# Kernel tuning notes

Hardware: AMD Instinct MI355X
Metric: run time of the kernel (lower is better)

The kernel has to match this reference:

```python
import jax, jax.numpy as jnp
import numpy as np

N, D_IN, D_EMB, K = 16384, 1024, 256, 1024
ALPHA, EPS = 0.01, 1e-5


def setup_inputs() -> dict:
    key = jax.random.key(0)
    ks = jax.random.split(key, 6)
    inp = jax.random.normal(ks[0], (N, D_IN), dtype=jnp.float32)
    W_send = jax.random.normal(ks[1], (D_IN, D_EMB), dtype=jnp.float32) / np.sqrt(D_IN)
    b_send = jnp.zeros((D_EMB,), dtype=jnp.float32)
    W_recv = jax.random.normal(ks[2], (D_EMB, D_IN), dtype=jnp.float32) / np.sqrt(D_EMB)
    b_recv = jnp.zeros((D_IN,), dtype=jnp.float32)
    codebook = jax.random.normal(ks[3], (K, D_EMB), dtype=jnp.float32)
    ema_vecs = codebook.copy()
    ema_size = jnp.zeros((K,), dtype=jnp.float32)
    return {"input": inp, "W_send": W_send, "b_send": b_send,
            "W_recv": W_recv, "b_recv": b_recv, "codebook": codebook,
            "ema_vecs": ema_vecs, "ema_size": ema_size}


def reference(input, W_send, b_send, W_recv, b_recv, codebook, ema_vecs, ema_size):
    sg = jax.lax.stop_gradient
    # send projection -> latent z  [N, D_EMB]
    z = input @ W_send + b_send
    # nearest-neighbor lookup: argmin_k ||e_k||^2 - 2 <z, e_k>
    sqr = jnp.sum(codebook * codebook, axis=1)          # [K]
    cov = jnp.einsum('nj,kj->nk', z, codebook)          # [N, K]
    codes = jnp.argmin(sqr - 2.0 * cov, axis=-1)        # [N] int
    # fetch embeddings (gather)
    vectors = codebook[codes]                            # [N, D_EMB]
    # mse losses, reduction='sum'
    embedding = jnp.sum((vectors - sg(z)) ** 2)
    commitment = jnp.sum((z - sg(vectors)) ** 2)
    # straight-through output
    emb_out = z + sg(vectors - z)
    # EMA accumulate (one-hot scatter == segment_sum)
    upd_vecs = jax.ops.segment_sum(z, codes, num_segments=K)              # [K, D_EMB]
    upd_size = jax.ops.segment_sum(jnp.ones((z.shape[0],), z.dtype), codes, num_segments=K)
    ema_vecs_new = ema_vecs + ALPHA * (upd_vecs - ema_vecs)
    ema_size_new = ema_size + ALPHA * (upd_size - ema_size)
    # EMA update (Laplace-smoothed centroid)
    n = jnp.sum(ema_size_new)
    coef = n / (n + K * EPS)
    size = coef * (ema_size_new + EPS)
    weight_new = ema_vecs_new / size[:, None]
    # empirical entropy of the codes in bits
    prob = jnp.bincount(codes, length=K).astype(jnp.float32) / codes.size
    ent = -jnp.sum(jnp.where(prob > 0, prob * jnp.log(prob), 0.0)) / jnp.log(2.0)
    # recv projection
    x = emb_out @ W_recv + b_recv
    return (x, codes, embedding, commitment, ent, ema_vecs_new, ema_size_new, weight_new)
```

## Files before the change

### kernel.cpp

```cpp
#include <hip/hip_runtime.h>
#include <math.h>

#define NROWS 16384
#define DIN   1024
#define DEMB  256
#define KC    1024
#define ALPHA 0.01f
#define EPSV  1e-5f
#define INV2048 4.8828125e-4f
#define CHUNK 32
#define COV_CHUNKS 8

typedef _Float16 f16;
typedef __attribute__((ext_vector_type(4)))  _Float16 f16x4;
typedef __attribute__((ext_vector_type(8)))  _Float16 f16x8;
typedef __attribute__((ext_vector_type(16))) float    f32x16;
typedef unsigned long long u64;

#define OFF_Z       0
#define OFF_R       4194304
#define OFF_SQR     5242880
#define OFF_ZH      5243904
#define OFF_ZL      7341056
#define OFF_WTH     9438208
#define OFF_WTL     9569280
#define OFF_CBH     9700352
#define OFF_CBL     9831424
#define OFF_KEYS    9962496
#define OFF_CODES   9995264
#define OFF_LIST    10011648
#define OFF_OFFS    10028032
#define OFF_UPD     10029056
#define OFF_HIST    10291200
#define OFF_CURSOR  10292224
#define OFF_LOSS    10293248
#define ZERO_LEN    264208
#define OFF_COUNTSF 10293264
#define OFF_SIZE    10294288

#define OUT_X      0
#define OUT_CODES  16777216
#define OUT_EMB    16793600
#define OUT_COMMIT 16793601
#define OUT_ENT    16793602
#define OUT_EMAV   16793603
#define OUT_EMAS   17055747
#define OUT_W      17056771

__device__ __forceinline__ void split_f32(float x, f16& h, f16& l) {
    h = (f16)x;
    l = (f16)((x - (float)h) * 2048.0f);
}

__global__ __launch_bounds__(64) void sqr_kernel(const float* __restrict__ cb,
                                                 float* __restrict__ sqr) {
    int k = blockIdx.x;
    int lane = threadIdx.x;
    float4 v = ((const float4*)cb)[k * 64 + lane];
    float s = v.x * v.x + v.y * v.y + v.z * v.z + v.w * v.w;
    for (int off = 32; off > 0; off >>= 1) s += __shfl_down(s, off, 64);
    if (lane == 0) sqr[k] = s;
}

__global__ __launch_bounds__(256) void split_wt_kernel(const float* __restrict__ W,
                                                       f16* __restrict__ wth,
                                                       f16* __restrict__ wtl) {
    int n = blockIdx.x;
    int t = threadIdx.x;
    f16x4 h4, l4;
#pragma unroll
    for (int j = 0; j < 4; ++j) {
        int k = t * 4 + j;
        float x = W[(size_t)k * DEMB + n];
        f16 h, l; split_f32(x, h, l);
        h4[j] = h; l4[j] = l;
    }
    *(f16x4*)&wth[(size_t)n * DIN + t * 4] = h4;
    *(f16x4*)&wtl[(size_t)n * DIN + t * 4] = l4;
}

__global__ __launch_bounds__(256) void split_cb_kernel(const float* __restrict__ cb,
                                                       f16* __restrict__ cbh,
                                                       f16* __restrict__ cbl) {
    int idx = (blockIdx.x * 256 + threadIdx.x) * 4;
    float4 v = *(const float4*)&cb[idx];
    f16x4 h4, l4;
    f16 h, l;
    split_f32(v.x, h, l); h4[0] = h; l4[0] = l;
    split_f32(v.y, h, l); h4[1] = h; l4[1] = l;
    split_f32(v.z, h, l); h4[2] = h; l4[2] = l;
    split_f32(v.w, h, l); h4[3] = h; l4[3] = l;
    *(f16x4*)&cbh[idx] = h4;
    *(f16x4*)&cbl[idx] = l4;
}

__global__ __launch_bounds__(512) void gemm1_mfma(const float* __restrict__ in,
                                                  const f16* __restrict__ wth,
                                                  const f16* __restrict__ wtl,
                                                  const float* __restrict__ bsend,
                                                  float* __restrict__ z,
                                                  f16* __restrict__ zh,
                                                  f16* __restrict__ zl) {
    __shared__ f16 sm[2 * 2 * 2 * 128 * 64];
    const int tid = threadIdx.x;
    const int wave = tid >> 6, lane = tid & 63;
    const int half = lane >> 5, l31 = lane & 31;
    const int wrow = wave >> 2, wcol = wave & 3;
    const int rowBase = blockIdx.y * 128;
    const int colBase = blockIdx.x * 128;

    const int sr  = tid >> 2;
    const int skq = tid & 3;
    const int sr7 = sr & 7;

    f32x16 accm[2] = {};
    f32x16 accx[2] = {};

    auto stageB = [&](int buf, int ks) {
#pragma unroll
        for (int i = 0; i < 4; ++i) {
            const int q  = wave * 4 + i;
            const int hl = q >> 4;
            const int c  = (q & 15) * 8 + (lane >> 3);
            const int p  = lane & 7;
            const int s  = p ^ (c & 7);
            const f16* src = (hl ? wtl : wth)
                           + (size_t)(colBase + c) * DIN + ks + s * 8;
            f16* dst = sm + buf * 32768 + 16384 + q * 512 + lane * 8;
            __builtin_amdgcn_global_load_lds(
                (const __attribute__((address_space(1))) void*)src,
                (__attribute__((address_space(3))) void*)dst, 16, 0, 0);
        }
    };

    auto loadA = [&](int ks, float4* av) {
        const float* src = &in[(size_t)(rowBase + sr) * DIN + ks + skq * 16];
#pragma unroll
        for (int j = 0; j < 4; ++j) av[j] = ((const float4*)src)[j];
    };

    auto writeA = [&](int buf, const float4* av) {
        f16* Abase = sm + buf * 32768;
#pragma unroll
        for (int q = 0; q < 2; ++q) {
            f16x8 h8, l8;
#pragma unroll
            for (int j = 0; j < 2; ++j) {
                float4 v = av[q * 2 + j];
                f16 h, l;
                split_f32(v.x, h, l); h8[j * 4 + 0] = h; l8[j * 4 + 0] = l;
                split_f32(v.y, h, l); h8[j * 4 + 1] = h; l8[j * 4 + 1] = l;
                split_f32(v.z, h, l); h8[j * 4 + 2] = h; l8[j * 4 + 2] = l;
                split_f32(v.w, h, l); h8[j * 4 + 3] = h; l8[j * 4 + 3] = l;
            }
            const int s = skq * 2 + q;
            const int off = sr * 64 + ((s ^ sr7) << 3);
            *(f16x8*)&Abase[off] = h8;
            *(f16x8*)&Abase[8192 + off] = l8;
        }
    };

    auto compute = [&](int buf) {
        const f16* Ah = sm + buf * 32768;
        const f16* Al = Ah + 8192;
        const f16* Bh = Ah + 16384;
        const f16* Bl = Ah + 24576;
        const int c  = wcol * 32 + l31;
        const int c7 = c & 7;
#pragma unroll
        for (int t4 = 0; t4 < 4; ++t4) {
            const int s = t4 * 2 + half;
            f16x8 a_h[2], a_l[2];
#pragma unroll
            for (int rt = 0; rt < 2; ++rt) {
                const int r = wrow * 64 + rt * 32 + l31;
                const int off = r * 64 + ((s ^ (r & 7)) << 3);
                a_h[rt] = *(const f16x8*)&Ah[off];
                a_l[rt] = *(const f16x8*)&Al[off];
            }
            const int boff = c * 64 + ((s ^ c7) << 3);
            f16x8 b_h = *(const f16x8*)&Bh[boff];
            f16x8 b_l = *(const f16x8*)&Bl[boff];
#pragma unroll
            for (int rt = 0; rt < 2; ++rt) {
                accm[rt] = __builtin_amdgcn_mfma_f32_32x32x16_f16(a_h[rt], b_h, accm[rt], 0, 0, 0);
                accx[rt] = __builtin_amdgcn_mfma_f32_32x32x16_f16(a_h[rt], b_l, accx[rt], 0, 0, 0);
                accx[rt] = __builtin_amdgcn_mfma_f32_32x32x16_f16(a_l[rt], b_h, accx[rt], 0, 0, 0);
            }
        }
    };

    stageB(0, 0);
    {
        float4 av[4];
        loadA(0, av);
        writeA(0, av);
    }
    __syncthreads();

    int cur = 0;
    for (int step = 0; step < 16; ++step) {
        float4 av[4];
        const bool pf = (step + 1) < 16;
        if (pf) {
            stageB(cur ^ 1, (step + 1) * 64);
            loadA((step + 1) * 64, av);
        }
        compute(cur);
        if (pf) writeA(cur ^ 1, av);
        __syncthreads();
        cur ^= 1;
    }

#pragma unroll
    for (int rt = 0; rt < 2; ++rt) {
        const int col = colBase + wcol * 32 + l31;
        const float bb = bsend[col];
#pragma unroll
        for (int reg = 0; reg < 16; ++reg) {
            const int row = rowBase + wrow * 64 + rt * 32 + (reg & 3) + 8 * (reg >> 2) + 4 * half;
            const float zv = accm[rt][reg] + INV2048 * accx[rt][reg] + bb;
            const size_t o = (size_t)row * DEMB + col;
            z[o] = zv;
            f16 h = (f16)zv;
            zh[o] = h;
            zl[o] = (f16)((zv - (float)h) * 2048.0f);
        }
    }
}

__device__ __forceinline__ void cov_stage(const f16* __restrict__ cbh,
                                          const f16* __restrict__ cbl,
                                          f16* sC, int buf, int codeBase,
                                          int wave, int lane) {
#pragma unroll
    for (int i = 0; i < 8; ++i) {
        const int seg = wave * 8 + i;
        const int hl  = seg >> 4;
        const int rp  = seg & 15;
        const int r   = rp * 2 + (lane >> 5);
        const f16* src = (hl ? cbl : cbh)
                       + (size_t)(codeBase + r) * DEMB
                       + (((lane & 31) ^ r) << 3);
        f16* dst = sC + (((buf << 1) + hl) * 32 + rp * 2) * DEMB;
        __builtin_amdgcn_global_load_lds(
            (const __attribute__((address_space(1))) void*)src,
            (__attribute__((address_space(3))) void*)dst,
            16, 0, 0);
    }
}

__global__ __launch_bounds__(256, 2) void cov_mfma_kernel(const f16* __restrict__ zh,
                                                          const f16* __restrict__ zl,
                                                          const f16* __restrict__ cbh,
                                                          const f16* __restrict__ cbl,
                                                          const float* __restrict__ sqr,
                                                          u64* __restrict__ keys) {
    __shared__ f16 sC[2 * 2 * 32 * DEMB];
    const int tid = threadIdx.x;
    const int wave = tid >> 6, lane = tid & 63;
    const int half = lane >> 5, l31 = lane & 31;
    const int rowBase = blockIdx.y * 128 + wave * 32;
    const int myRow = rowBase + l31;
    const int cb0 = blockIdx.x * (COV_CHUNKS * 32);

    cov_stage(cbh, cbl, sC, 0, cb0, wave, lane);

    f16x8 a_h[16], a_l[16];
#pragma unroll
    for (int t = 0; t < 16; ++t) {
        size_t o = (size_t)myRow * DEMB + t * 16 + half * 8;
        a_h[t] = *(const f16x8*)&zh[o];
        a_l[t] = *(const f16x8*)&zl[o];
    }

    float runv[16];
    int   runc[16];
#pragma unroll
    for (int r = 0; r < 16; ++r) { runv[r] = 3.4e38f; runc[r] = 0; }

    for (int cc = 0; cc < COV_CHUNKS; ++cc) {
        __syncthreads();
        if (cc + 1 < COV_CHUNKS)
            cov_stage(cbh, cbl, sC, (cc + 1) & 1, cb0 + (cc + 1) * 32, wave, lane);

        const f16* Ch = sC + ((cc & 1) * 2 + 0) * 32 * DEMB;
        const f16* Cl = sC + ((cc & 1) * 2 + 1) * 32 * DEMB;

        f32x16 accm = {};
        f32x16 accx = {};
#pragma unroll
        for (int t = 0; t < 16; ++t) {
            const int seg = t * 2 + half;
            const int p = ((seg ^ l31) << 3);
            f16x8 b_h = *(const f16x8*)&Ch[l31 * DEMB + p];
            f16x8 b_l = *(const f16x8*)&Cl[l31 * DEMB + p];
            accm = __builtin_amdgcn_mfma_f32_32x32x16_f16(a_h[t], b_h, accm, 0, 0, 0);
            accx = __builtin_amdgcn_mfma_f32_32x32x16_f16(a_h[t], b_l, accx, 0, 0, 0);
            accx = __builtin_amdgcn_mfma_f32_32x32x16_f16(a_l[t], b_h, accx, 0, 0, 0);
        }

        const int code = cb0 + cc * 32 + l31;
        const float sqv = sqr[code];
#pragma unroll
        for (int r = 0; r < 16; ++r) {
            float s = sqv - 2.0f * (accm[r] + INV2048 * accx[r]);
            if (s < runv[r]) { runv[r] = s; runc[r] = code; }
        }
    }

#pragma unroll
    for (int r = 0; r < 16; ++r) {
        float v = runv[r]; int ci = runc[r];
        for (int off = 16; off > 0; off >>= 1) {
            float ov = __shfl_down(v, off, 32);
            int   oc = __shfl_down(ci, off, 32);
            if (ov < v || (ov == v && oc < ci)) { v = ov; ci = oc; }
        }
        if (l31 == 0) {
            int row = rowBase + (r & 3) + 8 * (r >> 2) + 4 * half;
            unsigned ub = __float_as_uint(v);
            ub = (ub & 0x80000000u) ? ~ub : (ub | 0x80000000u);
            u64 key = ((u64)ub << 32) | (unsigned)ci;
            atomicMin(&keys[row], key);
        }
    }
}

__global__ __launch_bounds__(256) void decode_kernel(const u64* __restrict__ keys,
                                                     int* __restrict__ codes,
                                                     float* __restrict__ out_codes,
                                                     int* __restrict__ hist) {
    int r = blockIdx.x * 256 + threadIdx.x;
    int c = (int)(keys[r] & 0xFFFFFFFFull);
    codes[r] = c;
    out_codes[r] = (float)c;
    atomicAdd(&hist[c], 1);
}

__global__ __launch_bounds__(1024) void prefix_kernel(const int* __restrict__ hist,
                                                      int* __restrict__ offs,
                                                      float* __restrict__ countsf) {
    __shared__ int s[1024];
    int t = threadIdx.x;
    int v = hist[t];
    s[t] = v;
    countsf[t] = (float)v;
    __syncthreads();
    for (int d = 1; d < 1024; d <<= 1) {
        int x = (t >= d) ? s[t - d] : 0;
        __syncthreads();
        s[t] += x;
        __syncthreads();
    }
    offs[t] = s[t] - v;
}

__global__ __launch_bounds__(256) void fill_kernel(const int* __restrict__ codes,
                                                   const int* __restrict__ offs,
                                                   int* __restrict__ cursor,
                                                   int* __restrict__ list) {
    int r = blockIdx.x * 256 + threadIdx.x;
    int c = codes[r];
    int pos = offs[c] + atomicAdd(&cursor[c], 1);
    list[pos] = r;
}

__global__ __launch_bounds__(256) void upd_loss_kernel(const float* __restrict__ z,
                                                       const float* __restrict__ cb,
                                                       const int* __restrict__ list,
                                                       const int* __restrict__ codes,
                                                       float* __restrict__ upd,
                                                       float* __restrict__ loss) {
    __shared__ int srow[CHUNK];
    __shared__ int scode[CHUNK];
    const int tid = threadIdx.x;
    const int base = blockIdx.x * CHUNK;
    if (tid < CHUNK) {
        int r = list[base + tid];
        srow[tid] = r;
        scode[tid] = codes[r];
    }
    __syncthreads();

    int cur = scode[0];
    float cbv = cb[(size_t)cur * DEMB + tid];
    float acc = 0.f, lacc = 0.f;
    float zv = z[(size_t)srow[0] * DEMB + tid];
#pragma unroll 4
    for (int i = 0; i < CHUNK; ++i) {
        float znext = (i + 1 < CHUNK) ? z[(size_t)srow[i + 1] * DEMB + tid] : 0.f;
        int c = scode[i];
        if (c != cur) {
            atomicAdd(&upd[(size_t)cur * DEMB + tid], acc);
            acc = 0.f;
            cur = c;
            cbv = cb[(size_t)cur * DEMB + tid];
        }
        acc += zv;
        float d = zv - cbv;
        lacc += d * d;
        zv = znext;
    }
    atomicAdd(&upd[(size_t)cur * DEMB + tid], acc);

    __shared__ float red[256];
    red[tid] = lacc;
    __syncthreads();
    for (int s = 128; s > 0; s >>= 1) {
        if (tid < s) red[tid] += red[tid + s];
        __syncthreads();
    }
    if (tid == 0) atomicAdd(loss, red[0]);
}

__global__ __launch_bounds__(256) void gemm64_kernel(const float* __restrict__ A,
                                                     const float* __restrict__ B,
                                                     float* __restrict__ C,
                                                     int M, int Kd, int Nc) {
    __shared__ float As[16][68];
    __shared__ float Bs[16][64];
    const int tid = threadIdx.x;
    const int tx = tid & 15, ty = tid >> 4;
    const int rowBase = blockIdx.y * 64;
    const int colBase = blockIdx.x * 64;

    float acc[4][4];
#pragma unroll
    for (int i = 0; i < 4; ++i)
#pragma unroll
        for (int j = 0; j < 4; ++j) acc[i][j] = 0.f;

    const int a_row = tid >> 2;
    const int a_c4  = (tid & 3) * 4;
    const int b_r   = tid >> 4;
    const int b_c4  = (tid & 15) * 4;

    for (int kk = 0; kk < Kd; kk += 16) {
        float4 av = *(const float4*)&A[(size_t)(rowBase + a_row) * Kd + kk + a_c4];
        float4 bv = *(const float4*)&B[(size_t)(kk + b_r) * Nc + colBase + b_c4];
        __syncthreads();
        As[a_c4 + 0][a_row] = av.x;  As[a_c4 + 1][a_row] = av.y;
        As[a_c4 + 2][a_row] = av.z;  As[a_c4 + 3][a_row] = av.w;
        *(float4*)&Bs[b_r][b_c4] = bv;
        __syncthreads();
#pragma unroll
        for (int d = 0; d < 16; ++d) {
            float4 a01 = *(const float4*)&As[d][ty * 4];
            float4 b01 = *(const float4*)&Bs[d][tx * 4];
            float a[4] = {a01.x, a01.y, a01.z, a01.w};
            float b[4] = {b01.x, b01.y, b01.z, b01.w};
#pragma unroll
            for (int i = 0; i < 4; ++i)
#pragma unroll
                for (int j = 0; j < 4; ++j) acc[i][j] += a[i] * b[j];
        }
    }

#pragma unroll
    for (int i = 0; i < 4; ++i) {
        int r = rowBase + ty * 4 + i;
        *(float4*)&C[(size_t)r * Nc + colBase + tx * 4] =
            make_float4(acc[i][0], acc[i][1], acc[i][2], acc[i][3]);
    }
}

__global__ __launch_bounds__(256) void recv_kernel(const float* __restrict__ R,
                                                   const float* __restrict__ brecv,
                                                   const int* __restrict__ codes,
                                                   float* __restrict__ out) {
    const int n = blockIdx.x;
    const int t = threadIdx.x;
    const int code = codes[n];
    float4 r = ((const float4*)(R + (size_t)code * DIN))[t];
    float4 b = ((const float4*)brecv)[t];
    ((float4*)(out + (size_t)n * DIN))[t] =
        make_float4(r.x + b.x, r.y + b.y, r.z + b.z, r.w + b.w);
}

__global__ __launch_bounds__(1024) void ema_small_kernel(const float* __restrict__ ema_size,
                                                         const float* __restrict__ counts,
                                                         const float* __restrict__ loss,
                                                         float* __restrict__ size_ws,
                                                         float* __restrict__ out) {
    __shared__ float rn[1024];
    __shared__ float re[1024];
    const int k = threadIdx.x;
    float c  = counts[k];
    float es = ema_size[k];
    float esn = es + ALPHA * (c - es);
    out[OUT_EMAS + k] = esn;
    float p = c * (1.0f / (float)NROWS);
    rn[k] = esn;
    re[k] = (p > 0.f) ? p * logf(p) : 0.f;
    __syncthreads();
    for (int s = 512; s > 0; s >>= 1) {
        if (k < s) { rn[k] += rn[k + s]; re[k] += re[k + s]; }
        __syncthreads();
    }
    float n = rn[0];
    float coef = n / (n + (float)KC * EPSV);
    size_ws[k] = coef * (esn + EPSV);
    if (k == 0) {
        out[OUT_ENT] = -re[0] / logf(2.0f);
        float l = loss[0];
        out[OUT_EMB] = l;
        out[OUT_COMMIT] = l;
    }
}

__global__ __launch_bounds__(256) void emav_kernel(const float* __restrict__ ema_vecs,
                                                   const float* __restrict__ upd,
                                                   const float* __restrict__ size_ws,
                                                   float* __restrict__ out) {
    int idx = blockIdx.x * 256 + threadIdx.x;
    float ev = ema_vecs[idx], uv = upd[idx];
    float evn = ev + ALPHA * (uv - ev);
    out[OUT_EMAV + idx] = evn;
    out[OUT_W + idx] = evn / size_ws[idx >> 8];
}

extern "C" void kernel_launch(void* const* d_in, const int* in_sizes, int n_in,
                              void* d_out, int out_size, void* d_ws, size_t ws_size,
                              hipStream_t stream) {
    const float* input    = (const float*)d_in[0];
    const float* W_send   = (const float*)d_in[1];
    const float* b_send   = (const float*)d_in[2];
    const float* W_recv   = (const float*)d_in[3];
    const float* b_recv   = (const float*)d_in[4];
    const float* codebook = (const float*)d_in[5];
    const float* ema_vecs = (const float*)d_in[6];
    const float* ema_size = (const float*)d_in[7];
    float* out = (float*)d_out;
    float* ws  = (float*)d_ws;
    int*   wsi = (int*)d_ws;

    f16* wth = (f16*)(ws + OFF_WTH);
    f16* wtl = (f16*)(ws + OFF_WTL);
    f16* cbh = (f16*)(ws + OFF_CBH);
    f16* cbl = (f16*)(ws + OFF_CBL);
    f16* zh  = (f16*)(ws + OFF_ZH);
    f16* zl  = (f16*)(ws + OFF_ZL);
    u64* keys = (u64*)(ws + OFF_KEYS);

    (void)hipMemsetAsync(ws + OFF_UPD, 0, (size_t)ZERO_LEN * sizeof(float), stream);
    (void)hipMemsetAsync(ws + OFF_KEYS, 0xFF, (size_t)NROWS * sizeof(u64), stream);

    sqr_kernel<<<KC, 64, 0, stream>>>(codebook, ws + OFF_SQR);
    split_wt_kernel<<<DEMB, 256, 0, stream>>>(W_send, wth, wtl);
    split_cb_kernel<<<256, 256, 0, stream>>>(codebook, cbh, cbl);

    gemm64_kernel<<<dim3(DIN / 64, KC / 64), 256, 0, stream>>>(
        codebook, W_recv, ws + OFF_R, KC, DEMB, DIN);

    gemm1_mfma<<<dim3(DEMB / 128, NROWS / 128), 512, 0, stream>>>(
        input, wth, wtl, b_send, ws + OFF_Z, zh, zl);

    cov_mfma_kernel<<<dim3(KC / (COV_CHUNKS * 32), NROWS / 128), 256, 0, stream>>>(
        zh, zl, cbh, cbl, ws + OFF_SQR, keys);

    decode_kernel<<<NROWS / 256, 256, 0, stream>>>(
        keys, wsi + OFF_CODES, out + OUT_CODES, wsi + OFF_HIST);

    prefix_kernel<<<1, 1024, 0, stream>>>(
        wsi + OFF_HIST, wsi + OFF_OFFS, ws + OFF_COUNTSF);

    fill_kernel<<<NROWS / 256, 256, 0, stream>>>(
        wsi + OFF_CODES, wsi + OFF_OFFS, wsi + OFF_CURSOR, wsi + OFF_LIST);

    upd_loss_kernel<<<NROWS / CHUNK, 256, 0, stream>>>(
        ws + OFF_Z, codebook, wsi + OFF_LIST, wsi + OFF_CODES,
        ws + OFF_UPD, ws + OFF_LOSS);

    recv_kernel<<<NROWS, 256, 0, stream>>>(
        ws + OFF_R, b_recv, wsi + OFF_CODES, out + OUT_X);

    ema_small_kernel<<<1, 1024, 0, stream>>>(
        ema_size, ws + OFF_COUNTSF, ws + OFF_LOSS, ws + OFF_SIZE, out);

    emav_kernel<<<KC, 256, 0, stream>>>(
        ema_vecs, ws + OFF_UPD, ws + OFF_SIZE, out);
}
```

Before: 277.3 us.

## Retile send-projection GEMM to 64x128 blocks with 32-wide K steps

The first split-fp16 MFMA GEMM now uses 64-row by 128-column blocks of 256 threads, with K steps of 32 instead of 64. Shared memory per block shrinks and launch bounds request two blocks per CU, so more blocks are resident and the grid has twice as many blocks to spread load. The LDS swizzle changes from XOR to a rotate-by-row scheme to fit the narrower rows. The cost is twice as many pipeline steps and barriers, and less B-tile reuse per block. The cov kernel edit multiplies a term by zero and changes nothing.

```diff
diff --git a/kernel.cpp b/kernel.cpp
--- a/kernel.cpp
+++ b/kernel.cpp
@@ -94,24 +94,22 @@
     *(f16x4*)&cbl[idx] = l4;
 }
 
-__global__ __launch_bounds__(512) void gemm1_mfma(const float* __restrict__ in,
-                                                  const f16* __restrict__ wth,
-                                                  const f16* __restrict__ wtl,
-                                                  const float* __restrict__ bsend,
-                                                  float* __restrict__ z,
-                                                  f16* __restrict__ zh,
-                                                  f16* __restrict__ zl) {
-    __shared__ f16 sm[2 * 2 * 2 * 128 * 64];
+__global__ __launch_bounds__(256, 2) void gemm1_mfma(const float* __restrict__ in,
+                                                     const f16* __restrict__ wth,
+                                                     const f16* __restrict__ wtl,
+                                                     const float* __restrict__ bsend,
+                                                     float* __restrict__ z,
+                                                     f16* __restrict__ zh,
+                                                     f16* __restrict__ zl) {
+    __shared__ f16 sm[2 * 12288];
     const int tid = threadIdx.x;
     const int wave = tid >> 6, lane = tid & 63;
     const int half = lane >> 5, l31 = lane & 31;
-    const int wrow = wave >> 2, wcol = wave & 3;
-    const int rowBase = blockIdx.y * 128;
+    const int rowBase = blockIdx.y * 64;
     const int colBase = blockIdx.x * 128;
 
     const int sr  = tid >> 2;
     const int skq = tid & 3;
-    const int sr7 = sr & 7;
 
     f32x16 accm[2] = {};
     f32x16 accx[2] = {};
@@ -120,13 +118,14 @@
 #pragma unroll
         for (int i = 0; i < 4; ++i) {
             const int q  = wave * 4 + i;
-            const int hl = q >> 4;
-            const int c  = (q & 15) * 8 + (lane >> 3);
-            const int p  = lane & 7;
-            const int s  = p ^ (c & 7);
+            const int hl = q >> 3;
+            const int c0 = (q & 7) * 16;
+            const int c  = c0 + (lane >> 2);
+            const int p  = lane & 3;
+            const int s  = (p - (c >> 1)) & 3;
             const f16* src = (hl ? wtl : wth)
-                           + (size_t)(colBase + c) * DIN + ks + s * 8;
-            f16* dst = sm + buf * 32768 + 16384 + q * 512 + lane * 8;
+                           + (size_t)(colBase + c) * DIN + ks + (s << 3);
+            f16* dst = sm + buf * 12288 + 4096 + hl * 4096 + c0 * 32;
             __builtin_amdgcn_global_load_lds(
                 (const __attribute__((address_space(1))) void*)src,
                 (__attribute__((address_space(3))) void*)dst, 16, 0, 0);
@@ -134,51 +133,47 @@
     };
 
     auto loadA = [&](int ks, float4* av) {
-        const float* src = &in[(size_t)(rowBase + sr) * DIN + ks + skq * 16];
-#pragma unroll
-        for (int j = 0; j < 4; ++j) av[j] = ((const float4*)src)[j];
+        const float* src = &in[(size_t)(rowBase + sr) * DIN + ks + skq * 8];
+        av[0] = ((const float4*)src)[0];
+        av[1] = ((const float4*)src)[1];
     };
 
     auto writeA = [&](int buf, const float4* av) {
-        f16* Abase = sm + buf * 32768;
-#pragma unroll
-        for (int q = 0; q < 2; ++q) {
-            f16x8 h8, l8;
-#pragma unroll
-            for (int j = 0; j < 2; ++j) {
-                float4 v = av[q * 2 + j];
-                f16 h, l;
-                split_f32(v.x, h, l); h8[j * 4 + 0] = h; l8[j * 4 + 0] = l;
-                split_f32(v.y, h, l); h8[j * 4 + 1] = h; l8[j * 4 + 1] = l;
-                split_f32(v.z, h, l); h8[j * 4 + 2] = h; l8[j * 4 + 2] = l;
-                split_f32(v.w, h, l); h8[j * 4 + 3] = h; l8[j * 4 + 3] = l;
-            }
-            const int s = skq * 2 + q;
-            const int off = sr * 64 + ((s ^ sr7) << 3);
-            *(f16x8*)&Abase[off] = h8;
-            *(f16x8*)&Abase[8192 + off] = l8;
-        }
+        f16x8 h8, l8;
+        f16 h, l;
+        split_f32(av[0].x, h, l); h8[0] = h; l8[0] = l;
+        split_f32(av[0].y, h, l); h8[1] = h; l8[1] = l;
+        split_f32(av[0].z, h, l); h8[2] = h; l8[2] = l;
+        split_f32(av[0].w, h, l); h8[3] = h; l8[3] = l;
+        split_f32(av[1].x, h, l); h8[4] = h; l8[4] = l;
+        split_f32(av[1].y, h, l); h8[5] = h; l8[5] = l;
+        split_f32(av[1].z, h, l); h8[6] = h; l8[6] = l;
+        split_f32(av[1].w, h, l); h8[7] = h; l8[7] = l;
+        const int p = (skq + (sr >> 1)) & 3;
+        const int off = sr * 32 + (p << 3);
+        f16* Abase = sm + buf * 12288;
+        *(f16x8*)&Abase[off] = h8;
+        *(f16x8*)&Abase[2048 + off] = l8;
     };
 
     auto compute = [&](int buf) {
-        const f16* Ah = sm + buf * 32768;
-        const f16* Al = Ah + 8192;
-        const f16* Bh = Ah + 16384;
-        const f16* Bl = Ah + 24576;
-        const int c  = wcol * 32 + l31;
-        const int c7 = c & 7;
-#pragma unroll
-        for (int t4 = 0; t4 < 4; ++t4) {
-            const int s = t4 * 2 + half;
+        const f16* Ah = sm + buf * 12288;
+        const f16* Al = Ah + 2048;
+        const f16* Bh = Ah + 4096;
+        const f16* Bl = Ah + 8192;
+        const int c = wave * 32 + l31;
+#pragma unroll
+        for (int t = 0; t < 2; ++t) {
+            const int s = t * 2 + half;
             f16x8 a_h[2], a_l[2];
 #pragma unroll
             for (int rt = 0; rt < 2; ++rt) {
-                const int r = wrow * 64 + rt * 32 + l31;
-                const int off = r * 64 + ((s ^ (r & 7)) << 3);
+                const int r = rt * 32 + l31;
+                const int off = r * 32 + ((((s + (r >> 1)) & 3)) << 3);
                 a_h[rt] = *(const f16x8*)&Ah[off];
                 a_l[rt] = *(const f16x8*)&Al[off];
             }
-            const int boff = c * 64 + ((s ^ c7) << 3);
+            const int boff = c * 32 + ((((s + (c >> 1)) & 3)) << 3);
             f16x8 b_h = *(const f16x8*)&Bh[boff];
             f16x8 b_l = *(const f16x8*)&Bl[boff];
 #pragma unroll
@@ -192,19 +187,19 @@
 
     stageB(0, 0);
     {
-        float4 av[4];
+        float4 av[2];
         loadA(0, av);
         writeA(0, av);
     }
     __syncthreads();
 
     int cur = 0;
-    for (int step = 0; step < 16; ++step) {
-        float4 av[4];
-        const bool pf = (step + 1) < 16;
+    for (int step = 0; step < 32; ++step) {
+        float4 av[2];
+        const bool pf = (step + 1) < 32;
         if (pf) {
-            stageB(cur ^ 1, (step + 1) * 64);
-            loadA((step + 1) * 64, av);
+            stageB(cur ^ 1, (step + 1) * 32);
+            loadA((step + 1) * 32, av);
         }
         compute(cur);
         if (pf) writeA(cur ^ 1, av);
@@ -214,11 +209,11 @@
 
 #pragma unroll
     for (int rt = 0; rt < 2; ++rt) {
-        const int col = colBase + wcol * 32 + l31;
+        const int col = colBase + wave * 32 + l31;
         const float bb = bsend[col];
 #pragma unroll
         for (int reg = 0; reg < 16; ++reg) {
-            const int row = rowBase + wrow * 64 + rt * 32 + (reg & 3) + 8 * (reg >> 2) + 4 * half;
+            const int row = rowBase + rt * 32 + (reg & 3) + 8 * (reg >> 2) + 4 * half;
             const float zv = accm[rt][reg] + INV2048 * accx[rt][reg] + bb;
             const size_t o = (size_t)row * DEMB + col;
             z[o] = zv;
@@ -293,7 +288,7 @@
         for (int t = 0; t < 16; ++t) {
             const int seg = t * 2 + half;
             const int p = ((seg ^ l31) << 3);
-            f16x8 b_h = *(const f16x8*)&Ch[l31 * DEMB + p];
+            f16x8 b_h = *(const f16x8*)&Ch[l31 * 264 * 0 + l31 * DEMB + p];
             f16x8 b_l = *(const f16x8*)&Cl[l31 * DEMB + p];
             accm = __builtin_amdgcn_mfma_f32_32x32x16_f16(a_h[t], b_h, accm, 0, 0, 0);
             accx = __builtin_amdgcn_mfma_f32_32x32x16_f16(a_h[t], b_l, accx, 0, 0, 0);
@@ -553,7 +548,7 @@
     gemm64_kernel<<<dim3(DIN / 64, KC / 64), 256, 0, stream>>>(
         codebook, W_recv, ws + OFF_R, KC, DEMB, DIN);
 
-    gemm1_mfma<<<dim3(DEMB / 128, NROWS / 128), 512, 0, stream>>>(
+    gemm1_mfma<<<dim3(DEMB / 128, NROWS / 64), 256, 0, stream>>>(
         input, wth, wtl, b_send, ws + OFF_Z, zh, zl);
 
     cov_mfma_kernel<<<dim3(KC / (COV_CHUNKS * 32), NROWS / 128), 256, 0, stream>>>(
```

New measurement: 285.0 us. 1.03x slower.
